# Optimization experiments

Hardware: AMD Instinct MI355X
Metric: run time of the kernel (lower is better)

## Reference

```python
import jax, jax.numpy as jnp
import numpy as np

B, T, C, H = 4, 4096, 512, 64

def setup_inputs() -> dict:
    key = jax.random.key(0)
    kx, kk, kq, kv = jax.random.split(key, 4)
    return {
        "x": jax.random.normal(kx, (B, T, C), dtype=jnp.float32),
        "Wk": jax.random.normal(kk, (C, H), dtype=jnp.float32) * (C ** -0.5),
        "Wq": jax.random.normal(kq, (C, H), dtype=jnp.float32) * (C ** -0.5),
        "Wv": jax.random.normal(kv, (C, H), dtype=jnp.float32) * (C ** -0.5),
    }

def reference(x, Wk, Wq, Wv):
    # x: [B, T, C]; bias-free projections to head_size H
    k = x @ Wk  # [B, T, H]
    q = x @ Wq  # [B, T, H]
    v = x @ Wv  # [B, T, H]
    channels = x.shape[-1]
    # NOTE: original scales by channels**-0.5 (embedding dim), not head_size
    scale = jnp.asarray(channels, x.dtype) ** -0.5
    wei = jnp.einsum("bth,bsh->bts", q, k) * scale  # [B, T, T]
    t = x.shape[1]
    causal = jnp.tril(jnp.ones((t, t), dtype=bool))
    wei = jnp.where(causal, wei, -jnp.inf)
    wei = jax.nn.softmax(wei, axis=-1)
    out = jnp.einsum("bts,bsh->bth", wei, v)  # [B, T, H]
    return out
```

## Files before the change

### kernel.cpp

```cpp
#include <hip/hip_runtime.h>


typedef __attribute__((ext_vector_type(8))) __bf16 bf16x8;
typedef __attribute__((ext_vector_type(8))) unsigned short u16x8;
typedef __attribute__((ext_vector_type(4))) float f32x4;

#define B_ 4
#define T_ 4096
#define C_ 512
#define H_ 64
#define BT (B_ * T_)

#define QSCALE (0.04419417382415922f * 1.4426950408889634f)

__device__ __forceinline__ unsigned short f2bf(float f) {
    unsigned int u = __builtin_bit_cast(unsigned int, f);
    u += 0x7fffu + ((u >> 16) & 1u);
    return (unsigned short)(u >> 16);
}

__device__ __forceinline__ unsigned int pkbf(float hi, float lo) {
    return __builtin_amdgcn_perm(__builtin_bit_cast(unsigned int, hi),
                                 __builtin_bit_cast(unsigned int, lo), 0x07060302u);
}

__device__ __forceinline__ float bf2f_lo(unsigned int u) {
    return __builtin_bit_cast(float, u << 16);
}
__device__ __forceinline__ float bf2f_hi(unsigned int u) {
    return __builtin_bit_cast(float, u & 0xffff0000u);
}

__device__ __forceinline__ f32x4 mfma16(bf16x8 a, bf16x8 b, f32x4 c) {
    return __builtin_amdgcn_mfma_f32_16x16x32_bf16(a, b, c, 0, 0, 0);
}

__global__ __launch_bounds__(256) void wt_kernel(const float* __restrict__ Wk,
                                                 const float* __restrict__ Wq,
                                                 const float* __restrict__ Wv,
                                                 unsigned short* __restrict__ Wtp) {
    int gid = blockIdx.x * 256 + threadIdx.x;
    int fidx = gid >> 9;
    int li = gid & 511;
    int lane = li >> 3, j = li & 7;
    int m3 = fidx / 64;
    int rem = fidx & 63;
    int nt = rem >> 4, kc = rem & 15;
    int h = nt * 16 + (lane & 15);
    int c = kc * 32 + (lane >> 4) * 8 + j;
    const float* W = (m3 == 0) ? Wk : ((m3 == 1) ? Wq : Wv);
    Wtp[gid] = f2bf(W[c * H_ + h]);
}

__global__ __launch_bounds__(256, 3) void proj_kernel(const float* __restrict__ x,
                                                      const unsigned short* __restrict__ Wtp,
                                                      unsigned short* __restrict__ Kf,
                                                      unsigned short* __restrict__ Qf,
                                                      unsigned short* __restrict__ Vf) {
    __shared__ __align__(16) char smem[2 * 64 * 52 * 4];
    float* Mg = (float*)smem;
    unsigned short* Ks_l = (unsigned short*)smem;
    unsigned short* Qs_l = Ks_l + 32 * 68;
    unsigned short* Vt_l = Qs_l + 32 * 68;

    const int tid = threadIdx.x;
    const int t0 = blockIdx.x * 32;
    const int wave = tid >> 6;
    const int ws = wave & 1;
    const int wh = wave >> 1;
    const int lane = tid & 63;
    const int lane15 = lane & 15;
    const int quad = lane >> 4;

    f32x4 acc[12];
#pragma unroll
    for (int i = 0; i < 12; ++i) acc[i] = (f32x4){0.f, 0.f, 0.f, 0.f};

    const float* xrow = x + (long)(t0 + ws * 16 + lane15) * C_;
    const unsigned short* wbase = Wtp + lane * 8;

    bf16x8 wf[12];
    float4 xa0, xa1;
    {
        const int kc0 = wh * 8;
        xa0 = *(const float4*)(xrow + kc0 * 32 + quad * 8);
        xa1 = *(const float4*)(xrow + kc0 * 32 + quad * 8 + 4);
#pragma unroll
        for (int i = 0; i < 12; ++i)
            wf[i] = *(const bf16x8*)(wbase + ((i * 16 + kc0) << 9));
    }

#pragma unroll
    for (int kk = 0; kk < 8; ++kk) {
        const int kc = wh * 8 + kk;
        u16x8 t;
        t[0] = f2bf(xa0.x); t[1] = f2bf(xa0.y); t[2] = f2bf(xa0.z); t[3] = f2bf(xa0.w);
        t[4] = f2bf(xa1.x); t[5] = f2bf(xa1.y); t[6] = f2bf(xa1.z); t[7] = f2bf(xa1.w);
        bf16x8 a = __builtin_bit_cast(bf16x8, t);
        if (kk < 7) {
            xa0 = *(const float4*)(xrow + (kc + 1) * 32 + quad * 8);
            xa1 = *(const float4*)(xrow + (kc + 1) * 32 + quad * 8 + 4);
        }
#pragma unroll
        for (int i = 0; i < 12; ++i) {
            acc[i] = mfma16(a, wf[i], acc[i]);
            if (kk < 7)
                wf[i] = *(const bf16x8*)(wbase + ((i * 16 + kc + 1) << 9));
        }
    }

    if (wh == 1) {
        float* mg = Mg + (ws * 64 + lane) * 52;
#pragma unroll
        for (int i = 0; i < 12; ++i) *(f32x4*)(mg + i * 4) = acc[i];
    }
    __syncthreads();
    if (wh == 0) {
        const float* mg = Mg + (ws * 64 + lane) * 52;
#pragma unroll
        for (int i = 0; i < 12; ++i) acc[i] += *(const f32x4*)(mg + i * 4);
    }
    __syncthreads();

    if (wh == 0) {
#pragma unroll
        for (int nt = 0; nt < 4; ++nt) {
            int col = nt * 16 + lane15;
#pragma unroll
            for (int r = 0; r < 4; ++r) {
                int row_l = ws * 16 + quad * 4 + r;
                Ks_l[row_l * 68 + col] = f2bf(acc[0 * 4 + nt][r]);
                Qs_l[row_l * 68 + col] = f2bf(acc[1 * 4 + nt][r] * QSCALE);
                Vt_l[col * 34 + row_l] = f2bf(acc[2 * 4 + nt][r]);
            }
        }
    }
    __syncthreads();

    const int b = t0 >> 12;
    const int tloc = t0 & 4095;
    const int st = wave >> 1, kk = wave & 1;
    const long gs = (long)(b * 256 + (tloc >> 4) + st);
    bf16x8 kv = *(const bf16x8*)&Ks_l[(st * 16 + lane15) * 68 + kk * 32 + quad * 8];
    *(bf16x8*)&Kf[(gs * 2 + kk) * 512 + lane * 8] = kv;
    bf16x8 qv = *(const bf16x8*)&Qs_l[(st * 16 + lane15) * 68 + kk * 32 + quad * 8];
    *(bf16x8*)&Qf[(gs * 2 + kk) * 512 + lane * 8] = qv;
    const int hf = wave;
    const int vkk = (tloc >> 5) & 1;
    bf16x8 vv = *(const bf16x8*)&Vt_l[(hf * 16 + lane15) * 34 + quad * 8];
    const long sb = (long)(b * 64 + (tloc >> 6));
    *(bf16x8*)&Vf[(sb * 8 + hf * 2 + vkk) * 512 + lane * 8] = vv;
}

#define PSP 72

__global__ __launch_bounds__(256, 3) void attn_kernel(const unsigned short* __restrict__ Qf,
                                                      const unsigned short* __restrict__ Kf,
                                                      const unsigned short* __restrict__ Vf,
                                                      unsigned short* __restrict__ Opb,
                                                      float* __restrict__ lp,
                                                      float* __restrict__ out) {
    __shared__ __align__(16) unsigned short Ps[8 * 16 * PSP];

    const int tid = threadIdx.x;
    const int wave = tid >> 6;
    const int lane = tid & 63;
    const int lane15 = lane & 15;
    const int quad = lane >> 4;
    const int b = blockIdx.y;

    const int z = 287 - blockIdx.x;
    int g = (int)((__builtin_sqrtf((float)z + 1.0f) - 1.0f) * 0.5f);
    while (4 * (g + 1) * (g + 2) <= z) ++g;
    while (4 * g * (g + 1) > z) --g;
    const int idx = z - 4 * g * (g + 1);
    const int qt = g * 8 + idx / (g + 1);
    const int chunk = idx % (g + 1);
    const int ntt = min(8, qt + 1 - chunk * 8);
    const int t0k = chunk * 8;

    const long gs_q = (long)(b * 256 + qt * 4 + wave);
    const unsigned short* qb = Qf + gs_q * 1024 + lane * 8;
    const bf16x8 qf0 = *(const bf16x8*)qb;
    const bf16x8 qf1 = *(const bf16x8*)(qb + 512);

    f32x4 o_acc[4];
    f32x4 l_vec = (f32x4){0.f, 0.f, 0.f, 0.f};
#pragma unroll
    for (int hf = 0; hf < 4; ++hf) o_acc[hf] = (f32x4){0.f, 0.f, 0.f, 0.f};

    bf16x8 kf[8], vf[8];
    {
        const unsigned short* kb = Kf + (long)(b * 256 + t0k * 4) * 1024 + lane * 8;
        const unsigned short* vb = Vf + (long)(b * 64 + t0k) * 4096 + lane * 8;
#pragma unroll
        for (int ct = 0; ct < 4; ++ct) {
            kf[ct * 2 + 0] = *(const bf16x8*)(kb + ct * 1024);
            kf[ct * 2 + 1] = *(const bf16x8*)(kb + ct * 1024 + 512);
        }
#pragma unroll
        for (int f = 0; f < 8; ++f) vf[f] = *(const bf16x8*)(vb + f * 512);
    }

#pragma unroll 2
    for (int t = 0; t < ntt; ++t) {
        const int kc = t0k + t;
        const bool more = (t + 1 < ntt);
        const unsigned short* kbn = Kf + (long)(b * 256 + (kc + 1) * 4) * 1024 + lane * 8;
        const unsigned short* vbn = Vf + (long)(b * 64 + kc + 1) * 4096 + lane * 8;
        unsigned short* pw = Ps + ((wave << 1) | (t & 1)) * 16 * PSP;

        f32x4 st[4];
#pragma unroll
        for (int ct = 0; ct < 4; ++ct) {
            f32x4 zz = (f32x4){0.f, 0.f, 0.f, 0.f};
            zz = mfma16(kf[ct * 2 + 0], qf0, zz);
            zz = mfma16(kf[ct * 2 + 1], qf1, zz);
            st[ct] = zz;
        }

        if (more) {
#pragma unroll
            for (int ct = 0; ct < 4; ++ct) {
                kf[ct * 2 + 0] = *(const bf16x8*)(kbn + ct * 1024);
                kf[ct * 2 + 1] = *(const bf16x8*)(kbn + ct * 1024 + 512);
            }
        }

        if (kc == qt) {
            const int qg = wave * 16 + lane15;
#pragma unroll
            for (int ct = 0; ct < 4; ++ct) {
                const int sb = ct * 16 + quad * 4;
#pragma unroll
                for (int r = 0; r < 4; ++r)
                    if (sb + r > qg) st[ct][r] = -3.0e38f;
            }
        }

#pragma unroll
        for (int ct = 0; ct < 4; ++ct) {
#pragma unroll
            for (int r = 0; r < 4; ++r)
                st[ct][r] = __builtin_amdgcn_exp2f(st[ct][r]);
            l_vec += st[ct];
        }

#pragma unroll
        for (int ct = 0; ct < 4; ++ct) {
            unsigned int w0 = pkbf(st[ct][1], st[ct][0]);
            unsigned int w1 = pkbf(st[ct][3], st[ct][2]);
            *(uint2*)&pw[lane15 * PSP + ct * 16 + quad * 4] = make_uint2(w0, w1);
        }

        bf16x8 pa0 = *(const bf16x8*)&pw[lane15 * PSP + quad * 8];
        bf16x8 pa1 = *(const bf16x8*)&pw[lane15 * PSP + 32 + quad * 8];
#pragma unroll
        for (int hf = 0; hf < 4; ++hf) {
            o_acc[hf] = mfma16(pa0, vf[hf * 2 + 0], o_acc[hf]);
            o_acc[hf] = mfma16(pa1, vf[hf * 2 + 1], o_acc[hf]);
        }

        if (more) {
#pragma unroll
            for (int f = 0; f < 8; ++f) vf[f] = *(const bf16x8*)(vbn + f * 512);
        }
    }

    float l_acc = (l_vec[0] + l_vec[1]) + (l_vec[2] + l_vec[3]);
    l_acc += __shfl_xor(l_acc, 16);
    l_acc += __shfl_xor(l_acc, 32);

    if ((qt >> 3) == 0) {
        float linv[4];
#pragma unroll
        for (int r = 0; r < 4; ++r) linv[r] = 1.0f / __shfl(l_acc, quad * 4 + r);
        float* o = out + ((long)b * T_ + qt * 64 + wave * 16) * H_;
#pragma unroll
        for (int hf = 0; hf < 4; ++hf)
#pragma unroll
            for (int r = 0; r < 4; ++r)
                o[(quad * 4 + r) * H_ + hf * 16 + lane15] = o_acc[hf][r] * linv[r];
    } else {
        const long pbase = ((long)(b * 64 + qt) * 8 + chunk) * 64;
        if (quad == 0) lp[pbase + wave * 16 + lane15] = l_acc;
        unsigned short* op = Opb + (pbase + wave * 16) * 64;
#pragma unroll
        for (int hf = 0; hf < 4; ++hf)
#pragma unroll
            for (int r = 0; r < 4; ++r)
                op[(quad * 4 + r) * 64 + hf * 16 + lane15] = f2bf(o_acc[hf][r]);
    }
}

__global__ __launch_bounds__(256) void merge_kernel(const unsigned short* __restrict__ Opb,
                                                    const float* __restrict__ lp,
                                                    float* __restrict__ out) {
    const int qt = 8 + blockIdx.x;
    const int b = blockIdx.y;
    const int nc = 1 + (qt >> 3);
    const int tid = threadIdx.x;
    const int row = tid >> 2;
    const int seg = (tid & 3) << 4;

    const long base = (long)(b * 64 + qt) * 8;
    float l = 0.f;
    f32x4 a[4];
#pragma unroll
    for (int j = 0; j < 4; ++j) a[j] = (f32x4){0.f, 0.f, 0.f, 0.f};

    for (int c = 0; c < nc; ++c) {
        l += lp[(base + c) * 64 + row];
        const unsigned short* op = Opb + ((base + c) * 64 + row) * 64 + seg;
        uint4 d0 = *(const uint4*)(op);
        uint4 d1 = *(const uint4*)(op + 8);
        a[0][0] += bf2f_lo(d0.x); a[0][1] += bf2f_hi(d0.x);
        a[0][2] += bf2f_lo(d0.y); a[0][3] += bf2f_hi(d0.y);
        a[1][0] += bf2f_lo(d0.z); a[1][1] += bf2f_hi(d0.z);
        a[1][2] += bf2f_lo(d0.w); a[1][3] += bf2f_hi(d0.w);
        a[2][0] += bf2f_lo(d1.x); a[2][1] += bf2f_hi(d1.x);
        a[2][2] += bf2f_lo(d1.y); a[2][3] += bf2f_hi(d1.y);
        a[3][0] += bf2f_lo(d1.z); a[3][1] += bf2f_hi(d1.z);
        a[3][2] += bf2f_lo(d1.w); a[3][3] += bf2f_hi(d1.w);
    }
    const float inv = 1.0f / l;
    float* o = out + ((long)b * T_ + qt * 64 + row) * H_ + seg;
#pragma unroll
    for (int j = 0; j < 4; ++j) *(f32x4*)(o + j * 4) = a[j] * inv;
}

extern "C" void kernel_launch(void* const* d_in, const int* in_sizes, int n_in,
                              void* d_out, int out_size, void* d_ws, size_t ws_size,
                              hipStream_t stream) {
    const float* x  = (const float*)d_in[0];
    const float* Wk = (const float*)d_in[1];
    const float* Wq = (const float*)d_in[2];
    const float* Wv = (const float*)d_in[3];
    float* out = (float*)d_out;

    char* ws = (char*)d_ws;
    unsigned short* Kf  = (unsigned short*)(ws);
    unsigned short* Qf  = (unsigned short*)(ws + (2u << 20));
    unsigned short* Vf  = (unsigned short*)(ws + (4u << 20));
    unsigned short* Wtp = (unsigned short*)(ws + (6u << 20));
    unsigned short* Opb = (unsigned short*)(ws + (8u << 20));
    float* lp = (float*)(ws + (26u << 20));

    wt_kernel<<<384, 256, 0, stream>>>(Wk, Wq, Wv, Wtp);
    proj_kernel<<<BT / 32, 256, 0, stream>>>(x, Wtp, Kf, Qf, Vf);
    attn_kernel<<<dim3(288, B_), 256, 0, stream>>>(Qf, Kf, Vf, Opb, lp, out);
    merge_kernel<<<dim3(56, B_), 256, 0, stream>>>(Opb, lp, out);
}
```

Before: 118.4 us.

## Double-buffer x loads, raise MFMA wave priority, and split merge across more blocks

The projection kernel now prefetches x two k-chunks ahead through a two-slot register buffer, so global load latency is hidden further ahead of use. MFMA sections in both the projection and attention kernels are wrapped in s_setprio(1)/s_setprio(0) so the scheduler favours waves issuing matrix work. The merge kernel launches twice as many blocks, each handling 32 rows with 8 lanes per row and one 16-byte load per row, which gives more parallelism for a small kernel. The costs are extra registers in the projection kernel and priority changes that may starve other waves.

```diff
diff --git a/kernel.cpp b/kernel.cpp
--- a/kernel.cpp
+++ b/kernel.cpp
@@ -80,11 +80,13 @@
     const unsigned short* wbase = Wtp + lane * 8;
 
     bf16x8 wf[12];
-    float4 xa0, xa1;
+    float4 xa0[2], xa1[2];
     {
         const int kc0 = wh * 8;
-        xa0 = *(const float4*)(xrow + kc0 * 32 + quad * 8);
-        xa1 = *(const float4*)(xrow + kc0 * 32 + quad * 8 + 4);
+        xa0[0] = *(const float4*)(xrow + kc0 * 32 + quad * 8);
+        xa1[0] = *(const float4*)(xrow + kc0 * 32 + quad * 8 + 4);
+        xa0[1] = *(const float4*)(xrow + (kc0 + 1) * 32 + quad * 8);
+        xa1[1] = *(const float4*)(xrow + (kc0 + 1) * 32 + quad * 8 + 4);
 #pragma unroll
         for (int i = 0; i < 12; ++i)
             wf[i] = *(const bf16x8*)(wbase + ((i * 16 + kc0) << 9));
@@ -93,20 +95,25 @@
 #pragma unroll
     for (int kk = 0; kk < 8; ++kk) {
         const int kc = wh * 8 + kk;
+        const int cur = kk & 1;
         u16x8 t;
-        t[0] = f2bf(xa0.x); t[1] = f2bf(xa0.y); t[2] = f2bf(xa0.z); t[3] = f2bf(xa0.w);
-        t[4] = f2bf(xa1.x); t[5] = f2bf(xa1.y); t[6] = f2bf(xa1.z); t[7] = f2bf(xa1.w);
+        t[0] = f2bf(xa0[cur].x); t[1] = f2bf(xa0[cur].y);
+        t[2] = f2bf(xa0[cur].z); t[3] = f2bf(xa0[cur].w);
+        t[4] = f2bf(xa1[cur].x); t[5] = f2bf(xa1[cur].y);
+        t[6] = f2bf(xa1[cur].z); t[7] = f2bf(xa1[cur].w);
         bf16x8 a = __builtin_bit_cast(bf16x8, t);
-        if (kk < 7) {
-            xa0 = *(const float4*)(xrow + (kc + 1) * 32 + quad * 8);
-            xa1 = *(const float4*)(xrow + (kc + 1) * 32 + quad * 8 + 4);
-        }
+        if (kk < 6) {
+            xa0[cur] = *(const float4*)(xrow + (kc + 2) * 32 + quad * 8);
+            xa1[cur] = *(const float4*)(xrow + (kc + 2) * 32 + quad * 8 + 4);
+        }
+        __builtin_amdgcn_s_setprio(1);
 #pragma unroll
         for (int i = 0; i < 12; ++i) {
             acc[i] = mfma16(a, wf[i], acc[i]);
             if (kk < 7)
                 wf[i] = *(const bf16x8*)(wbase + ((i * 16 + kc + 1) << 9));
         }
+        __builtin_amdgcn_s_setprio(0);
     }
 
     if (wh == 1) {
@@ -211,6 +218,7 @@
         unsigned short* pw = Ps + ((wave << 1) | (t & 1)) * 16 * PSP;
 
         f32x4 st[4];
+        __builtin_amdgcn_s_setprio(1);
 #pragma unroll
         for (int ct = 0; ct < 4; ++ct) {
             f32x4 zz = (f32x4){0.f, 0.f, 0.f, 0.f};
@@ -218,6 +226,7 @@
             zz = mfma16(kf[ct * 2 + 1], qf1, zz);
             st[ct] = zz;
         }
+        __builtin_amdgcn_s_setprio(0);
 
         if (more) {
 #pragma unroll
@@ -255,11 +264,13 @@
 
         bf16x8 pa0 = *(const bf16x8*)&pw[lane15 * PSP + quad * 8];
         bf16x8 pa1 = *(const bf16x8*)&pw[lane15 * PSP + 32 + quad * 8];
+        __builtin_amdgcn_s_setprio(1);
 #pragma unroll
         for (int hf = 0; hf < 4; ++hf) {
             o_acc[hf] = mfma16(pa0, vf[hf * 2 + 0], o_acc[hf]);
             o_acc[hf] = mfma16(pa1, vf[hf * 2 + 1], o_acc[hf]);
         }
+        __builtin_amdgcn_s_setprio(0);
 
         if (more) {
 #pragma unroll
@@ -296,37 +307,33 @@
 __global__ __launch_bounds__(256) void merge_kernel(const unsigned short* __restrict__ Opb,
                                                     const float* __restrict__ lp,
                                                     float* __restrict__ out) {
-    const int qt = 8 + blockIdx.x;
+    const int qt = 8 + (blockIdx.x >> 1);
+    const int rh = (blockIdx.x & 1) << 5;
     const int b = blockIdx.y;
     const int nc = 1 + (qt >> 3);
     const int tid = threadIdx.x;
-    const int row = tid >> 2;
-    const int seg = (tid & 3) << 4;
+    const int row = rh + (tid >> 3);
+    const int seg = (tid & 7) << 3;
 
     const long base = (long)(b * 64 + qt) * 8;
     float l = 0.f;
-    f32x4 a[4];
-#pragma unroll
-    for (int j = 0; j < 4; ++j) a[j] = (f32x4){0.f, 0.f, 0.f, 0.f};
-
+    f32x4 a0 = (f32x4){0.f, 0.f, 0.f, 0.f};
+    f32x4 a1 = (f32x4){0.f, 0.f, 0.f, 0.f};
+
+#pragma unroll 2
     for (int c = 0; c < nc; ++c) {
         l += lp[(base + c) * 64 + row];
         const unsigned short* op = Opb + ((base + c) * 64 + row) * 64 + seg;
-        uint4 d0 = *(const uint4*)(op);
-        uint4 d1 = *(const uint4*)(op + 8);
-        a[0][0] += bf2f_lo(d0.x); a[0][1] += bf2f_hi(d0.x);
-        a[0][2] += bf2f_lo(d0.y); a[0][3] += bf2f_hi(d0.y);
-        a[1][0] += bf2f_lo(d0.z); a[1][1] += bf2f_hi(d0.z);
-        a[1][2] += bf2f_lo(d0.w); a[1][3] += bf2f_hi(d0.w);
-        a[2][0] += bf2f_lo(d1.x); a[2][1] += bf2f_hi(d1.x);
-        a[2][2] += bf2f_lo(d1.y); a[2][3] += bf2f_hi(d1.y);
-        a[3][0] += bf2f_lo(d1.z); a[3][1] += bf2f_hi(d1.z);
-        a[3][2] += bf2f_lo(d1.w); a[3][3] += bf2f_hi(d1.w);
+        uint4 d = *(const uint4*)op;
+        a0[0] += bf2f_lo(d.x); a0[1] += bf2f_hi(d.x);
+        a0[2] += bf2f_lo(d.y); a0[3] += bf2f_hi(d.y);
+        a1[0] += bf2f_lo(d.z); a1[1] += bf2f_hi(d.z);
+        a1[2] += bf2f_lo(d.w); a1[3] += bf2f_hi(d.w);
     }
     const float inv = 1.0f / l;
     float* o = out + ((long)b * T_ + qt * 64 + row) * H_ + seg;
-#pragma unroll
-    for (int j = 0; j < 4; ++j) *(f32x4*)(o + j * 4) = a[j] * inv;
+    *(f32x4*)o = a0 * inv;
+    *(f32x4*)(o + 4) = a1 * inv;
 }
 
 extern "C" void kernel_launch(void* const* d_in, const int* in_sizes, int n_in,
@@ -349,5 +356,5 @@
     wt_kernel<<<384, 256, 0, stream>>>(Wk, Wq, Wv, Wtp);
     proj_kernel<<<BT / 32, 256, 0, stream>>>(x, Wtp, Kf, Qf, Vf);
     attn_kernel<<<dim3(288, B_), 256, 0, stream>>>(Qf, Kf, Vf, Opb, lp, out);
-    merge_kernel<<<dim3(56, B_), 256, 0, stream>>>(Opb, lp, out);
-}
+    merge_kernel<<<dim3(112, B_), 256, 0, stream>>>(Opb, lp, out);
+}
```

New measurement: 115.5 us (median of 2 runs). 1.02x faster.
